# Performance work log

Measured on AMD Instinct MI355X. Metric: run time of the kernel, lower is better.

Reference implementation:

```python
import jax, jax.numpy as jnp
import numpy as np
import math

B, L, D = 4, 4096, 64

def setup_inputs() -> dict:
    key = jax.random.key(0)
    kq, kk, kv = jax.random.split(key, 3)
    q = jax.random.normal(kq, (B, L, D), dtype=jnp.float32)
    k = jax.random.normal(kk, (B, L, D), dtype=jnp.float32)
    v = jax.random.normal(kv, (B, L, D), dtype=jnp.float32)
    return {"q": q, "k": k, "v": v}

def reference(q, k, v):
    d_model = k.shape[-1]
    # score[b,i,j] = <q_i, k_j> / sqrt(d)   -> [B, L, L]
    score = jnp.einsum('bid,bjd->bij', q, k) / math.sqrt(d_model)
    attn = jax.nn.softmax(score.astype(jnp.float32), axis=-1)
    # Faithful to source: output = (v^T @ attn)^T = attn^T @ v
    # output[b,j,d] = sum_i attn[b,i,j] * v[b,i,d]
    out = jnp.einsum('bij,bid->bjd', attn, v)
    return out
```

## Files before the change

kernel.cpp:

```cpp
#include <hip/hip_runtime.h>
#include <hip/hip_bf16.h>

#define LQ 4096
#define DD 64
#define NB 4
#define NTOT ((size_t)NB * LQ * DD)
#define NROW ((size_t)NB * LQ)
#define NJC 16

typedef __attribute__((ext_vector_type(4))) float f32x4;
typedef __attribute__((ext_vector_type(8))) short short8;
typedef __attribute__((ext_vector_type(4))) short short4v;
typedef __attribute__((ext_vector_type(2))) unsigned int uint2v;
typedef __attribute__((ext_vector_type(4))) unsigned short ushort4v;

static __device__ __forceinline__ unsigned short f2bf(float x) {
  __hip_bfloat16 h = __float2bfloat16(x);
  return __builtin_bit_cast(unsigned short, h);
}
static __device__ __forceinline__ float ex2(float x) { return __builtin_amdgcn_exp2f(x); }

static __device__ __forceinline__ f32x4 mfma16(short4v a, short4v b, f32x4 c) {
#if __has_builtin(__builtin_amdgcn_mfma_f32_16x16x16bf16_1k)
  return __builtin_amdgcn_mfma_f32_16x16x16bf16_1k(a, b, c, 0, 0, 0);
#else
  asm volatile("v_mfma_f32_16x16x16_bf16 %0, %1, %2, %0"
               : "+v"(c) : "v"(a), "v"(b));
  return c;
#endif
}

#define C1 0.18033688011112042f


__global__ __launch_bounds__(256) void prep_kernel(
    const float* __restrict__ q, const float* __restrict__ k,
    unsigned short* __restrict__ Qf, unsigned short* __restrict__ Kf)
{
  __shared__ __align__(16) unsigned short tile[64][72];
  const int bx = blockIdx.x;
  const int b = bx >> 6, s = bx & 63;
  const int tid = threadIdx.x;
  const int r = tid >> 2, c0 = (tid & 3) << 4;
  const int w = tid >> 6, lane = tid & 63;
  const int l15 = lane & 15, g = lane >> 4;
  const size_t rowbase = ((size_t)b * LQ + s * 64 + r) * DD + c0;
  const size_t bbase = (size_t)b * LQ * DD;

#pragma unroll
  for (int arr = 0; arr < 2; ++arr) {
    const float* src = arr ? k : q;
    unsigned short* dst = arr ? Kf : Qf;
    ushort4v o[4];
#pragma unroll
    for (int e = 0; e < 4; ++e) {
      const f32x4 x = *(const f32x4*)(src + rowbase + e * 4);
      o[e] = (ushort4v){ f2bf(x[0]), f2bf(x[1]), f2bf(x[2]), f2bf(x[3]) };
    }
    if (arr) __syncthreads();
#pragma unroll
    for (int e = 0; e < 4; ++e) *(ushort4v*)(&tile[r][c0 + e * 4]) = o[e];
    __syncthreads();
    const int T = s * 4 + w;
#pragma unroll
    for (int kh = 0; kh < 2; ++kh) {
      const unsigned short* pp = &tile[w * 16 + l15][kh * 32 + g * 8];
      const ushort4v lo = *(const ushort4v*)pp;
      const ushort4v hi = *(const ushort4v*)(pp + 4);
      unsigned short* od = dst + bbase + (((size_t)T * 2 + kh) * 64 + lane) * 8;
      *(ushort4v*)od = lo;
      *(ushort4v*)(od + 4) = hi;
    }
  }
}

__global__ __launch_bounds__(256) void stats_kernel(
    const unsigned short* __restrict__ Qf, const unsigned short* __restrict__ Kf,
    float* __restrict__ part_ls)
{
  const int bx = blockIdx.x;
  const int x = bx & 7, kk = bx >> 3;
  const int b = x >> 1;
  const int jc = ((x & 1) << 3) + (kk >> 4);
  const int it = kk & 15;
  const int tid = threadIdx.x, w = tid >> 6, lane = tid & 63;
  const int l15 = lane & 15, g = lane >> 4;
  const size_t bbase = (size_t)b * LQ * DD;
  const unsigned short* Qp = Qf + bbase;
  const unsigned short* Kp = Kf + bbase;

  short8 aq[4][2];
#pragma unroll
  for (int is = 0; is < 4; ++is)
#pragma unroll
    for (int kh = 0; kh < 2; ++kh) {
      const int T = it * 16 + w * 4 + is;
      aq[is][kh] = *(const short8*)(Qp + (((size_t)T * 2 + kh) * 64 + lane) * 8);
    }

  float ls[4][4];
#pragma unroll
  for (int is = 0; is < 4; ++is)
#pragma unroll
    for (int qq = 0; qq < 4; ++qq) ls[is][qq] = 0.f;

  const int J0 = jc * 16;
  short8 kf[3][2];
#pragma unroll
  for (int pb = 0; pb < 2; ++pb)
#pragma unroll
    for (int kh = 0; kh < 2; ++kh)
      kf[pb][kh] = *(const short8*)(Kp + (((size_t)(J0 + pb) * 2 + kh) * 64 + lane) * 8);

#pragma unroll
  for (int itr = 0; itr < 16; ++itr) {
    const int buf = itr % 3;
    if (itr + 2 < 16) {
      const int nb2 = (itr + 2) % 3;
#pragma unroll
      for (int kh = 0; kh < 2; ++kh)
        kf[nb2][kh] = *(const short8*)(Kp + (((size_t)(J0 + itr + 2) * 2 + kh) * 64 + lane) * 8);
    }
#pragma unroll
    for (int is = 0; is < 4; ++is) {
      f32x4 tt = __builtin_amdgcn_mfma_f32_16x16x32_bf16(
          aq[is][0], kf[buf][0], (f32x4){0.f, 0.f, 0.f, 0.f}, 0, 0, 0);
      tt = __builtin_amdgcn_mfma_f32_16x16x32_bf16(aq[is][1], kf[buf][1], tt, 0, 0, 0);
#pragma unroll
      for (int qq = 0; qq < 4; ++qq) ls[is][qq] += ex2(tt[qq] * C1);
    }
  }
#pragma unroll
  for (int mask = 1; mask <= 8; mask <<= 1)
#pragma unroll
    for (int is = 0; is < 4; ++is)
#pragma unroll
      for (int qq = 0; qq < 4; ++qq) ls[is][qq] += __shfl_xor(ls[is][qq], mask, 64);
  if (l15 == 0) {
#pragma unroll
    for (int is = 0; is < 4; ++is) {
      const int T = it * 16 + w * 4 + is;
#pragma unroll
      for (int qq = 0; qq < 4; ++qq)
        part_ls[(size_t)jc * NROW + b * LQ + T * 16 + g * 4 + qq] = ls[is][qq];
    }
  }
}

__global__ __launch_bounds__(256) void combine_kernel(
    const float* __restrict__ part_ls, const float* __restrict__ v,
    unsigned short* __restrict__ Vf)
{
  __shared__ __align__(16) unsigned short tile[64][72];
  const int bx = blockIdx.x;
  const int b = bx >> 6, s = bx & 63;
  const int tid = threadIdx.x;
  const int r = tid >> 2, c0 = (tid & 3) << 4;
  const int w = tid >> 6, lane = tid & 63;
  const int l15 = lane & 15, g = lane >> 4;
  const int row = b * LQ + s * 64 + r;

  float l = 0.f;
#pragma unroll
  for (int jc = 0; jc < NJC; ++jc) l += part_ls[(size_t)jc * NROW + row];
  const float sc = 1.0f / l;

  const size_t rowbase = (size_t)row * DD + c0;
#pragma unroll
  for (int e = 0; e < 4; ++e) {
    const f32x4 xv = *(const f32x4*)(v + rowbase + e * 4);
    ushort4v o = { f2bf(xv[0] * sc), f2bf(xv[1] * sc),
                   f2bf(xv[2] * sc), f2bf(xv[3] * sc) };
    *(ushort4v*)(&tile[r][c0 + e * 4]) = o;
  }
  __syncthreads();
  const int T = s * 4 + w;
  const size_t bbase = (size_t)b * LQ * DD;
#pragma unroll
  for (int dp = 0; dp < 2; ++dp) {
    ushort4v lo, hi;
#pragma unroll
    for (int c = 0; c < 4; ++c) {
      lo[c] = tile[w * 16 + g * 4 + c][(2 * dp) * 16 + l15];
      hi[c] = tile[w * 16 + g * 4 + c][(2 * dp + 1) * 16 + l15];
    }
    unsigned short* od = Vf + bbase + (((size_t)T * 2 + dp) * 64 + lane) * 8;
    *(ushort4v*)od = lo;
    *(ushort4v*)(od + 4) = hi;
  }
}

__global__ __launch_bounds__(512, 2) void attn_out_kernel(
    const unsigned short* __restrict__ Qf, const unsigned short* __restrict__ Kf,
    const unsigned short* __restrict__ Vf, float* __restrict__ out)
{
  __shared__ float red[8 * 4096];

  const int bx = blockIdx.x;
  const int x = bx & 7;
  const int b = x >> 1;
  const int jt = ((x & 1) << 5) + (bx >> 3);
  const int tid = threadIdx.x, w = tid >> 6, lane = tid & 63;
  const int l15 = lane & 15, g = lane >> 4;

  const size_t bbase = (size_t)b * LQ * DD;
  const unsigned short* Qp = Qf + bbase;
  const unsigned short* Kp = Kf + bbase;
  const unsigned short* Vp = Vf + bbase;

  short8 ka[4][2];
#pragma unroll
  for (int js = 0; js < 4; ++js)
#pragma unroll
    for (int kh = 0; kh < 2; ++kh) {
      const int JT = jt * 4 + js;
      ka[js][kh] = *(const short8*)(Kp + (((size_t)JT * 2 + kh) * 64 + lane) * 8);
    }

  f32x4 acc[4][4];
#pragma unroll
  for (int js = 0; js < 4; ++js)
#pragma unroll
    for (int ds = 0; ds < 4; ++ds) acc[js][ds] = (f32x4){0.f, 0.f, 0.f, 0.f};

  const int T0 = w * 32;
  short8 qb[3][2], vb[3][2];
#pragma unroll
  for (int pb = 0; pb < 2; ++pb) {
#pragma unroll
    for (int kh = 0; kh < 2; ++kh)
      qb[pb][kh] = *(const short8*)(Qp + (((size_t)(T0 + pb) * 2 + kh) * 64 + lane) * 8);
#pragma unroll
    for (int dp = 0; dp < 2; ++dp)
      vb[pb][dp] = *(const short8*)(Vp + (((size_t)(T0 + pb) * 2 + dp) * 64 + lane) * 8);
  }

#pragma unroll
  for (int itr = 0; itr < 32; ++itr) {
    const int buf = itr % 3;
    if (itr + 2 < 32) {
      const int nb2 = (itr + 2) % 3;
      const int Tn = T0 + itr + 2;
#pragma unroll
      for (int kh = 0; kh < 2; ++kh)
        qb[nb2][kh] = *(const short8*)(Qp + (((size_t)Tn * 2 + kh) * 64 + lane) * 8);
#pragma unroll
      for (int dp = 0; dp < 2; ++dp)
        vb[nb2][dp] = *(const short8*)(Vp + (((size_t)Tn * 2 + dp) * 64 + lane) * 8);
    }

    union VU { short8 s8; short4v s4[2]; } vu0, vu1;
    vu0.s8 = vb[buf][0];
    vu1.s8 = vb[buf][1];

    __builtin_amdgcn_s_setprio(1);
#pragma unroll
    for (int js = 0; js < 4; ++js) {
      f32x4 tt = __builtin_amdgcn_mfma_f32_16x16x32_bf16(
          qb[buf][0], ka[js][0], (f32x4){0.f, 0.f, 0.f, 0.f}, 0, 0, 0);
      tt = __builtin_amdgcn_mfma_f32_16x16x32_bf16(qb[buf][1], ka[js][1], tt, 0, 0, 0);
      const unsigned a0 = __builtin_bit_cast(unsigned, ex2(tt[0] * C1)) + 0x8000u;
      const unsigned a1 = __builtin_bit_cast(unsigned, ex2(tt[1] * C1)) + 0x8000u;
      const unsigned a2 = __builtin_bit_cast(unsigned, ex2(tt[2] * C1)) + 0x8000u;
      const unsigned a3 = __builtin_bit_cast(unsigned, ex2(tt[3] * C1)) + 0x8000u;
      uint2v uu;
      uu[0] = __builtin_amdgcn_perm(a1, a0, 0x07060302u);
      uu[1] = __builtin_amdgcn_perm(a3, a2, 0x07060302u);
      const short4v pa = __builtin_bit_cast(short4v, uu);
      acc[js][0] = mfma16(pa, vu0.s4[0], acc[js][0]);
      acc[js][1] = mfma16(pa, vu0.s4[1], acc[js][1]);
      acc[js][2] = mfma16(pa, vu1.s4[0], acc[js][2]);
      acc[js][3] = mfma16(pa, vu1.s4[1], acc[js][3]);
    }
    __builtin_amdgcn_s_setprio(0);
  }

  __syncthreads();
#pragma unroll
  for (int js = 0; js < 4; ++js)
#pragma unroll
    for (int ds = 0; ds < 4; ++ds)
#pragma unroll
      for (int qq = 0; qq < 4; ++qq)
        red[w * 4096 + (js * 16 + g * 4 + qq) * 64 + ds * 16 + l15] = acc[js][ds][qq];
  __syncthreads();
  {
    float* op = out + ((size_t)b * LQ + jt * 64) * DD;
    const int jj = tid >> 3;
    const int d0 = (tid & 7) << 3;
    f32x4 s0 = (f32x4){0.f, 0.f, 0.f, 0.f};
    f32x4 s1 = (f32x4){0.f, 0.f, 0.f, 0.f};
#pragma unroll
    for (int u = 0; u < 8; ++u) {
      const f32x4 t0 = *(const f32x4*)&red[u * 4096 + jj * 64 + d0];
      const f32x4 t1 = *(const f32x4*)&red[u * 4096 + jj * 64 + d0 + 4];
      s0[0] += t0[0]; s0[1] += t0[1]; s0[2] += t0[2]; s0[3] += t0[3];
      s1[0] += t1[0]; s1[1] += t1[1]; s1[2] += t1[2]; s1[3] += t1[3];
    }
    *(f32x4*)(op + jj * 64 + d0) = s0;
    *(f32x4*)(op + jj * 64 + d0 + 4) = s1;
  }
}

extern "C" void kernel_launch(void* const* d_in, const int* in_sizes, int n_in,
                              void* d_out, int out_size, void* d_ws, size_t ws_size,
                              hipStream_t stream) {
  const float* q = (const float*)d_in[0];
  const float* k = (const float*)d_in[1];
  const float* v = (const float*)d_in[2];

  unsigned short* Qf = (unsigned short*)d_ws;
  unsigned short* Kf = Qf + NTOT;
  unsigned short* Vf = Kf + NTOT;
  float* part_ls = (float*)(Vf + NTOT);
  float* outp = (float*)d_out;

  prep_kernel<<<NB * 64, 256, 0, stream>>>(q, k, Qf, Kf);
  stats_kernel<<<1024, 256, 0, stream>>>(Qf, Kf, part_ls);
  combine_kernel<<<NB * 64, 256, 0, stream>>>(part_ls, v, Vf);
  attn_out_kernel<<<256, 512, 0, stream>>>(Qf, Kf, Vf, outp);
}
```

Before: 51.57 us.

## Fold row normalizer into exponent via log-sum, convert V in prep kernel

V is now converted to bf16 in the prep kernel alongside Q and K, so the V conversion no longer has to wait for the softmax statistics. A small kernel sums the partial row sums and takes their log, and the attention kernel subtracts this per-row value inside the exp2 through an FMA, replacing the earlier scaling of V by 1/l. The combine kernel becomes much lighter. The cost is an extra per-row float load per iteration in the main loop and a log-domain normalizer, which slightly changes rounding.

New measurement: 50.72 us. No clear change (-1.6%).

```diff
diff --git a/kernel.cpp b/kernel.cpp
--- a/kernel.cpp
+++ b/kernel.cpp
@@ -35,39 +35,64 @@
 
 __global__ __launch_bounds__(256) void prep_kernel(
     const float* __restrict__ q, const float* __restrict__ k,
-    unsigned short* __restrict__ Qf, unsigned short* __restrict__ Kf)
+    const float* __restrict__ v,
+    unsigned short* __restrict__ Qf, unsigned short* __restrict__ Kf,
+    unsigned short* __restrict__ Vf)
 {
   __shared__ __align__(16) unsigned short tile[64][72];
   const int bx = blockIdx.x;
-  const int b = bx >> 6, s = bx & 63;
+  const int half = bx >> 8;
+  const int b = (bx & 255) >> 6, s = bx & 63;
   const int tid = threadIdx.x;
   const int r = tid >> 2, c0 = (tid & 3) << 4;
   const int w = tid >> 6, lane = tid & 63;
   const int l15 = lane & 15, g = lane >> 4;
   const size_t rowbase = ((size_t)b * LQ + s * 64 + r) * DD + c0;
   const size_t bbase = (size_t)b * LQ * DD;
-
-#pragma unroll
-  for (int arr = 0; arr < 2; ++arr) {
-    const float* src = arr ? k : q;
-    unsigned short* dst = arr ? Kf : Qf;
-    ushort4v o[4];
+  const int T = s * 4 + w;
+
+  if (half == 0) {
+#pragma unroll
+    for (int arr = 0; arr < 2; ++arr) {
+      const float* src = arr ? k : q;
+      unsigned short* dst = arr ? Kf : Qf;
+      ushort4v o[4];
+#pragma unroll
+      for (int e = 0; e < 4; ++e) {
+        const f32x4 x = *(const f32x4*)(src + rowbase + e * 4);
+        o[e] = (ushort4v){ f2bf(x[0]), f2bf(x[1]), f2bf(x[2]), f2bf(x[3]) };
+      }
+      if (arr) __syncthreads();
+#pragma unroll
+      for (int e = 0; e < 4; ++e) *(ushort4v*)(&tile[r][c0 + e * 4]) = o[e];
+      __syncthreads();
+#pragma unroll
+      for (int kh = 0; kh < 2; ++kh) {
+        const unsigned short* pp = &tile[w * 16 + l15][kh * 32 + g * 8];
+        const ushort4v lo = *(const ushort4v*)pp;
+        const ushort4v hi = *(const ushort4v*)(pp + 4);
+        unsigned short* od = dst + bbase + (((size_t)T * 2 + kh) * 64 + lane) * 8;
+        *(ushort4v*)od = lo;
+        *(ushort4v*)(od + 4) = hi;
+      }
+    }
+  } else {
 #pragma unroll
     for (int e = 0; e < 4; ++e) {
-      const f32x4 x = *(const f32x4*)(src + rowbase + e * 4);
-      o[e] = (ushort4v){ f2bf(x[0]), f2bf(x[1]), f2bf(x[2]), f2bf(x[3]) };
-    }
-    if (arr) __syncthreads();
-#pragma unroll
-    for (int e = 0; e < 4; ++e) *(ushort4v*)(&tile[r][c0 + e * 4]) = o[e];
+      const f32x4 xv = *(const f32x4*)(v + rowbase + e * 4);
+      ushort4v o = { f2bf(xv[0]), f2bf(xv[1]), f2bf(xv[2]), f2bf(xv[3]) };
+      *(ushort4v*)(&tile[r][c0 + e * 4]) = o;
+    }
     __syncthreads();
-    const int T = s * 4 + w;
-#pragma unroll
-    for (int kh = 0; kh < 2; ++kh) {
-      const unsigned short* pp = &tile[w * 16 + l15][kh * 32 + g * 8];
-      const ushort4v lo = *(const ushort4v*)pp;
-      const ushort4v hi = *(const ushort4v*)(pp + 4);
-      unsigned short* od = dst + bbase + (((size_t)T * 2 + kh) * 64 + lane) * 8;
+#pragma unroll
+    for (int dp = 0; dp < 2; ++dp) {
+      ushort4v lo, hi;
+#pragma unroll
+      for (int c = 0; c < 4; ++c) {
+        lo[c] = tile[w * 16 + g * 4 + c][(2 * dp) * 16 + l15];
+        hi[c] = tile[w * 16 + g * 4 + c][(2 * dp + 1) * 16 + l15];
+      }
+      unsigned short* od = Vf + bbase + (((size_t)T * 2 + dp) * 64 + lane) * 8;
       *(ushort4v*)od = lo;
       *(ushort4v*)(od + 4) = hi;
     }
@@ -147,52 +172,20 @@
   }
 }
 
-__global__ __launch_bounds__(256) void combine_kernel(
-    const float* __restrict__ part_ls, const float* __restrict__ v,
-    unsigned short* __restrict__ Vf)
+__global__ __launch_bounds__(256) void logify_kernel(
+    const float* __restrict__ part_ls, float* __restrict__ c2)
 {
-  __shared__ __align__(16) unsigned short tile[64][72];
-  const int bx = blockIdx.x;
-  const int b = bx >> 6, s = bx & 63;
-  const int tid = threadIdx.x;
-  const int r = tid >> 2, c0 = (tid & 3) << 4;
-  const int w = tid >> 6, lane = tid & 63;
-  const int l15 = lane & 15, g = lane >> 4;
-  const int row = b * LQ + s * 64 + r;
-
-  float l = 0.f;
-#pragma unroll
-  for (int jc = 0; jc < NJC; ++jc) l += part_ls[(size_t)jc * NROW + row];
-  const float sc = 1.0f / l;
-
-  const size_t rowbase = (size_t)row * DD + c0;
-#pragma unroll
-  for (int e = 0; e < 4; ++e) {
-    const f32x4 xv = *(const f32x4*)(v + rowbase + e * 4);
-    ushort4v o = { f2bf(xv[0] * sc), f2bf(xv[1] * sc),
-                   f2bf(xv[2] * sc), f2bf(xv[3] * sc) };
-    *(ushort4v*)(&tile[r][c0 + e * 4]) = o;
-  }
-  __syncthreads();
-  const int T = s * 4 + w;
-  const size_t bbase = (size_t)b * LQ * DD;
-#pragma unroll
-  for (int dp = 0; dp < 2; ++dp) {
-    ushort4v lo, hi;
-#pragma unroll
-    for (int c = 0; c < 4; ++c) {
-      lo[c] = tile[w * 16 + g * 4 + c][(2 * dp) * 16 + l15];
-      hi[c] = tile[w * 16 + g * 4 + c][(2 * dp + 1) * 16 + l15];
-    }
-    unsigned short* od = Vf + bbase + (((size_t)T * 2 + dp) * 64 + lane) * 8;
-    *(ushort4v*)od = lo;
-    *(ushort4v*)(od + 4) = hi;
-  }
+  const int x = blockIdx.x * 256 + threadIdx.x;
+  float s = 0.f;
+#pragma unroll
+  for (int jc = 0; jc < NJC; ++jc) s += part_ls[(size_t)jc * NROW + x];
+  c2[x] = __builtin_amdgcn_logf(s);
 }
 
 __global__ __launch_bounds__(512, 2) void attn_out_kernel(
     const unsigned short* __restrict__ Qf, const unsigned short* __restrict__ Kf,
-    const unsigned short* __restrict__ Vf, float* __restrict__ out)
+    const unsigned short* __restrict__ Vf, const float* __restrict__ c2,
+    float* __restrict__ out)
 {
   __shared__ float red[8 * 4096];
 
@@ -207,6 +200,7 @@
   const unsigned short* Qp = Qf + bbase;
   const unsigned short* Kp = Kf + bbase;
   const unsigned short* Vp = Vf + bbase;
+  const float* c2p = c2 + b * LQ + g * 4;
 
   short8 ka[4][2];
 #pragma unroll
@@ -225,6 +219,7 @@
 
   const int T0 = w * 32;
   short8 qb[3][2], vb[3][2];
+  f32x4 cb[3];
 #pragma unroll
   for (int pb = 0; pb < 2; ++pb) {
 #pragma unroll
@@ -233,6 +228,7 @@
 #pragma unroll
     for (int dp = 0; dp < 2; ++dp)
       vb[pb][dp] = *(const short8*)(Vp + (((size_t)(T0 + pb) * 2 + dp) * 64 + lane) * 8);
+    cb[pb] = *(const f32x4*)(c2p + (T0 + pb) * 16);
   }
 
 #pragma unroll
@@ -247,11 +243,13 @@
 #pragma unroll
       for (int dp = 0; dp < 2; ++dp)
         vb[nb2][dp] = *(const short8*)(Vp + (((size_t)Tn * 2 + dp) * 64 + lane) * 8);
+      cb[nb2] = *(const f32x4*)(c2p + Tn * 16);
     }
 
     union VU { short8 s8; short4v s4[2]; } vu0, vu1;
     vu0.s8 = vb[buf][0];
     vu1.s8 = vb[buf][1];
+    const f32x4 cc = cb[buf];
 
     __builtin_amdgcn_s_setprio(1);
 #pragma unroll
@@ -259,10 +257,10 @@
       f32x4 tt = __builtin_amdgcn_mfma_f32_16x16x32_bf16(
           qb[buf][0], ka[js][0], (f32x4){0.f, 0.f, 0.f, 0.f}, 0, 0, 0);
       tt = __builtin_amdgcn_mfma_f32_16x16x32_bf16(qb[buf][1], ka[js][1], tt, 0, 0, 0);
-      const unsigned a0 = __builtin_bit_cast(unsigned, ex2(tt[0] * C1)) + 0x8000u;
-      const unsigned a1 = __builtin_bit_cast(unsigned, ex2(tt[1] * C1)) + 0x8000u;
-      const unsigned a2 = __builtin_bit_cast(unsigned, ex2(tt[2] * C1)) + 0x8000u;
-      const unsigned a3 = __builtin_bit_cast(unsigned, ex2(tt[3] * C1)) + 0x8000u;
+      const unsigned a0 = __builtin_bit_cast(unsigned, ex2(__builtin_fmaf(tt[0], C1, -cc[0]))) + 0x8000u;
+      const unsigned a1 = __builtin_bit_cast(unsigned, ex2(__builtin_fmaf(tt[1], C1, -cc[1]))) + 0x8000u;
+      const unsigned a2 = __builtin_bit_cast(unsigned, ex2(__builtin_fmaf(tt[2], C1, -cc[2]))) + 0x8000u;
+      const unsigned a3 = __builtin_bit_cast(unsigned, ex2(__builtin_fmaf(tt[3], C1, -cc[3]))) + 0x8000u;
       uint2v uu;
       uu[0] = __builtin_amdgcn_perm(a1, a0, 0x07060302u);
       uu[1] = __builtin_amdgcn_perm(a3, a2, 0x07060302u);
@@ -313,10 +311,11 @@
   unsigned short* Kf = Qf + NTOT;
   unsigned short* Vf = Kf + NTOT;
   float* part_ls = (float*)(Vf + NTOT);
+  float* c2 = part_ls + (size_t)NJC * NROW;
   float* outp = (float*)d_out;
 
-  prep_kernel<<<NB * 64, 256, 0, stream>>>(q, k, Qf, Kf);
+  prep_kernel<<<512, 256, 0, stream>>>(q, k, v, Qf, Kf, Vf);
   stats_kernel<<<1024, 256, 0, stream>>>(Qf, Kf, part_ls);
-  combine_kernel<<<NB * 64, 256, 0, stream>>>(part_ls, v, Vf);
-  attn_out_kernel<<<256, 512, 0, stream>>>(Qf, Kf, Vf, outp);
-}
+  logify_kernel<<<(int)(NROW / 256), 256, 0, stream>>>(part_ls, c2);
+  attn_out_kernel<<<256, 512, 0, stream>>>(Qf, Kf, Vf, c2, outp);
+}
```
